# Optimization experiments

Measured on AMD Instinct MI355X. Metric: run time of the kernel, lower is better.

The kernel has to match this reference:

```python
import jax, jax.numpy as jnp
import numpy as np

D_MODEL = 1024
NUM_HEADS = 16
HEAD_DIM = D_MODEL // NUM_HEADS


def setup_inputs() -> dict:
    key = jax.random.key(0)
    ks = jax.random.split(key, 11)
    B, S = 2, 2048
    s = 1.0 / np.sqrt(D_MODEL)
    inp = {
        'q': jax.random.normal(ks[0], (B, S, D_MODEL), jnp.float32),
        'k': jax.random.normal(ks[1], (B, S, D_MODEL), jnp.float32),
        'v': jax.random.normal(ks[2], (B, S, D_MODEL), jnp.float32),
        'wq': jax.random.normal(ks[3], (D_MODEL, D_MODEL), jnp.float32) * s,
        'bq': jnp.zeros((D_MODEL,), jnp.float32),
        'wk': jax.random.normal(ks[4], (D_MODEL, D_MODEL), jnp.float32) * s,
        'bk': jnp.zeros((D_MODEL,), jnp.float32),
        'wv': jax.random.normal(ks[5], (D_MODEL, D_MODEL), jnp.float32) * s,
        'bv': jnp.zeros((D_MODEL,), jnp.float32),
        'wo': jax.random.normal(ks[6], (D_MODEL, D_MODEL), jnp.float32) * s,
        'bo': jnp.zeros((D_MODEL,), jnp.float32),
    }
    return inp


def _split_heads(x, B):
    # [B, S, D] -> [B, H, S, Hd]
    return x.reshape(B, -1, NUM_HEADS, HEAD_DIM).transpose(0, 2, 1, 3)


def reference(q, k, v, wq, bq, wk, bk, wv, bv, wo, bo):
    B = q.shape[0]
    qh = _split_heads(q @ wq + bq, B)
    kh = _split_heads(k @ wk + bk, B)
    vh = _split_heads(v @ wv + bv, B)
    scale = 1.0 / np.sqrt(HEAD_DIM).astype(np.float32)
    # [B, H, Sq, Sk]
    scores = jnp.einsum('bhqd,bhkd->bhqk', qh, kh) * scale
    probs = jax.nn.softmax(scores, axis=-1)
    out = jnp.einsum('bhqk,bhkd->bhqd', probs, vh)  # [B, H, Sq, Hd]
    out = out.transpose(0, 2, 1, 3).reshape(B, -1, D_MODEL)
    return out @ wo + bo
```

## Files before the change

### kernel.cpp

```cpp
#include <hip/hip_runtime.h>

typedef unsigned short u16;
typedef __bf16 bf16x8 __attribute__((ext_vector_type(8)));
typedef float    f32x4 __attribute__((ext_vector_type(4)));
typedef float   f32x16 __attribute__((ext_vector_type(16)));
typedef u16      u16x8 __attribute__((ext_vector_type(8)));
typedef u16      u16x4 __attribute__((ext_vector_type(4)));
typedef unsigned uint4v __attribute__((ext_vector_type(4)));

#define DM 1024
#define SQ 2048
#define HD 64
#define QSCALE 0.18033688f

#define SWZ8(row, ch) ((((ch) ^ ((row) & 7) ^ ((row) >> 3)) & 7))

__device__ __forceinline__ u16 f2bf(float f) {
    unsigned u = __builtin_bit_cast(unsigned, f);
    u += 0x7FFFu + ((u >> 16) & 1u);
    return (u16)(u >> 16);
}

__device__ __forceinline__ bf16x8 ldsbf(const u16* p) {
    return __builtin_bit_cast(bf16x8, *(const u16x8*)p);
}

__device__ __forceinline__ unsigned cvtpk(float a, float b) {
    unsigned r;
    asm("v_cvt_pk_bf16_f32 %0, %1, %2" : "=v"(r) : "v"(a), "v"(b));
    return r;
}

__device__ __forceinline__ void swap32(unsigned &a, unsigned &b) {
    asm volatile("v_permlane32_swap_b32 %0, %1" : "+v"(a), "+v"(b));
}

typedef __attribute__((address_space(3))) unsigned lds_u32_t;
typedef __attribute__((address_space(1))) const unsigned glob_u32_t;
__device__ __forceinline__ void gl_lds16(const u16* g, u16* l) {
    __builtin_amdgcn_global_load_lds((glob_u32_t*)g, (lds_u32_t*)l, 16, 0, 0);
}

__global__ __launch_bounds__(256) void prep_kernel(
    const float* __restrict__ q, const float* __restrict__ k,
    const float* __restrict__ v,
    const float* __restrict__ w0, const float* __restrict__ w1,
    const float* __restrict__ w2, const float* __restrict__ w3,
    u16* __restrict__ Qc, u16* __restrict__ Kc, u16* __restrict__ Vc,
    u16* __restrict__ t0, u16* __restrict__ t1,
    u16* __restrict__ t2, u16* __restrict__ t3)
{
    __shared__ float tile[32][33];
    const int bid = blockIdx.x;
    if (bid < 6144) {
        const int which = bid >> 11;
        const float* src = (which==0) ? q : (which==1) ? k : v;
        u16* dst         = (which==0) ? Qc : (which==1) ? Kc : Vc;
        const int off = ((bid & 2047) << 11) + threadIdx.x * 8;
        f32x4 x0 = *(const f32x4*)&src[off];
        f32x4 x1 = *(const f32x4*)&src[off + 4];
        u16x8 u;
#pragma unroll
        for (int e = 0; e < 4; ++e) { u[e] = f2bf(x0[e]); u[e+4] = f2bf(x1[e]); }
        *(u16x8*)&dst[off] = u;
    } else {
        const int t   = bid - 6144;
        const int z   = t >> 10;
        const int rem = t & 1023;
        const float* W = (z==0) ? w0 : (z==1) ? w1 : (z==2) ? w2 : w3;
        u16* T        = (z==0) ? t0 : (z==1) ? t1 : (z==2) ? t2 : t3;
        const float sc = (z==0) ? QSCALE : 1.0f;
        const int tx = threadIdx.x & 31, ty = threadIdx.x >> 5;
        const int n0 = (rem & 31) * 32, k0 = (rem >> 5) * 32;
#pragma unroll
        for (int i = 0; i < 4; ++i)
            tile[ty + 8*i][tx] = W[(size_t)(k0 + ty + 8*i)*DM + n0 + tx];
        __syncthreads();
#pragma unroll
        for (int i = 0; i < 4; ++i)
            T[(size_t)(n0 + ty + 8*i)*DM + k0 + tx] = f2bf(tile[tx][ty + 8*i] * sc);
    }
}

template<bool OF32, bool VTLAST>
__global__ __launch_bounds__(256) void gemm_kernel(
    const u16* __restrict__ a0, const u16* __restrict__ a1, const u16* __restrict__ a2,
    const u16* __restrict__ w0, const u16* __restrict__ w1, const u16* __restrict__ w2,
    const float* __restrict__ bi0, const float* __restrict__ bi1, const float* __restrict__ bi2,
    void* __restrict__ o0, void* __restrict__ o1, void* __restrict__ o2,
    float bscale0)
{
    __shared__ __align__(16) u16 As[2][128*64];
    __shared__ __align__(16) u16 Bs[2][128*64];

    const int cpx  = gridDim.x >> 3;
    const int wgid = (blockIdx.x & 7) * cpx + (blockIdx.x >> 3);
    const int z   = wgid >> 8;
    const int rem = wgid & 255;
    const int by  = rem >> 3, bx = rem & 7;

    const u16*  Ap  = (z==0) ? a0 : (z==1) ? a1 : a2;
    const u16*  Wp  = (z==0) ? w0 : (z==1) ? w1 : w2;
    const float* Bp = (z==0) ? bi0 : (z==1) ? bi1 : bi2;
    void* Op        = (z==0) ? o0 : (z==1) ? o1 : o2;
    const float bsc = (z==0) ? bscale0 : 1.0f;

    const int tid  = threadIdx.x;
    const int lane = tid & 63;
    const int wv   = tid >> 6;
    const int m0 = by * 128;
    const int n0 = bx * 128;
    const int wr = (wv >> 1) * 64;
    const int wc = (wv & 1) * 64;
    const int g  = lane >> 4;
    const int mm = lane & 15;

    const int l8 = lane >> 3;
    const int c8 = lane & 7;

    f32x4 acc[4][4];
#pragma unroll
    for (int i = 0; i < 4; ++i)
#pragma unroll
        for (int j = 0; j < 4; ++j) acc[i][j] = f32x4{0.f,0.f,0.f,0.f};

    auto stageA = [&](int kt, int buf) {
#pragma unroll
        for (int i = 0; i < 4; ++i) {
            const int row = i*32 + wv*8 + l8;
            const int ch  = c8 ^ (row & 7);
            gl_lds16(&Ap[(size_t)(m0+row)*DM + kt*64 + ch*8],
                     &As[buf][(i*32 + wv*8)*64]);
        }
    };
    auto stageW = [&](int kt, int buf) {
#pragma unroll
        for (int i = 0; i < 4; ++i) {
            const int row = i*32 + wv*8 + l8;
            const int ch  = c8 ^ (row & 7);
            gl_lds16(&Wp[(size_t)(n0+row)*DM + kt*64 + ch*8],
                     &Bs[buf][(i*32 + wv*8)*64]);
        }
    };

    stageA(0, 0); stageW(0, 0);

    for (int kt = 0; kt < 16; ++kt) {
        const int cur = kt & 1;
        if (kt < 15) { stageA(kt + 1, cur ^ 1); stageW(kt + 1, cur ^ 1); }
        if (kt < 15) asm volatile("s_waitcnt vmcnt(8)" ::: "memory");
        else         asm volatile("s_waitcnt vmcnt(0)" ::: "memory");
        __builtin_amdgcn_s_barrier();
        __builtin_amdgcn_sched_barrier(0);

#pragma unroll
        for (int ks = 0; ks < 2; ++ks) {
            bf16x8 af[4], bfr[4];
#pragma unroll
            for (int rt = 0; rt < 4; ++rt) {
                const int row = wr + rt*16 + mm;
                const int ch  = ks*4 + g;
                af[rt] = ldsbf(&As[cur][row*64 + ((ch ^ (row & 7)) << 3)]);
            }
#pragma unroll
            for (int ct = 0; ct < 4; ++ct) {
                const int row = wc + ct*16 + mm;
                const int ch  = ks*4 + g;
                bfr[ct] = ldsbf(&Bs[cur][row*64 + ((ch ^ (row & 7)) << 3)]);
            }
            __builtin_amdgcn_s_setprio(1);
#pragma unroll
            for (int rt = 0; rt < 4; ++rt)
#pragma unroll
                for (int ct = 0; ct < 4; ++ct)
                    acc[rt][ct] = __builtin_amdgcn_mfma_f32_16x16x32_bf16(
                        af[rt], bfr[ct], acc[rt][ct], 0, 0, 0);
            __builtin_amdgcn_s_setprio(0);
        }

        __builtin_amdgcn_sched_barrier(0);
        __builtin_amdgcn_s_barrier();
    }

    if (VTLAST && z == 2) {
#pragma unroll
        for (int ct = 0; ct < 4; ++ct) {
            const int col = n0 + wc + ct*16 + mm;
            const float bv = Bp[col] * bsc;
#pragma unroll
            for (int rt = 0; rt < 4; ++rt) {
                const int row0 = m0 + wr + rt*16 + g*4;
                const int bb = row0 >> 11, s = row0 & (SQ-1);
                u16x4 pk;
#pragma unroll
                for (int r = 0; r < 4; ++r) pk[r] = f2bf(acc[rt][ct][r] + bv);
                *(u16x4*)&((u16*)Op)[(size_t)(bb*DM + col)*SQ + s] = pk;
            }
        }
    } else {
#pragma unroll
        for (int ct = 0; ct < 4; ++ct) {
            const int col = n0 + wc + ct*16 + mm;
            const float bv = Bp[col] * bsc;
#pragma unroll
            for (int rt = 0; rt < 4; ++rt) {
#pragma unroll
                for (int r = 0; r < 4; ++r) {
                    const int row = m0 + wr + rt*16 + g*4 + r;
                    const float vv = acc[rt][ct][r] + bv;
                    if (OF32) ((float*)Op)[(size_t)row*DM + col] = vv;
                    else      ((u16*) Op)[(size_t)row*DM + col] = f2bf(vv);
                }
            }
        }
    }
}

__global__ __launch_bounds__(512) void attn_kernel(
    const u16* __restrict__ Q, const u16* __restrict__ K,
    const u16* __restrict__ Vt, u16* __restrict__ Z)
{
    __shared__ __align__(16) u16 Kl[2][64*64];
    __shared__ __align__(16) u16 Vl[2][64*64];

    const int tid  = threadIdx.x;
    const int lane = tid & 63;
    const int wid  = tid >> 6;
    const int c    = lane & 31;
    const int hi   = lane >> 5;
    const int srow = tid >> 3;
    const int c8   = tid & 7;

    const int wg = (blockIdx.x & 7) * 32 + (blockIdx.x >> 3);
    const int qt = wg & 7;
    const int hb = wg >> 3;
    const int h  = hb & 15;
    const int b  = hb >> 4;
    const int q0 = qt * 256;

    const size_t kbase = (size_t)(b*SQ)*DM + h*HD;
    const size_t vbase = (size_t)((b*16 + h)*HD)*SQ;

    bf16x8 qf[4];
    {
        const size_t qoff = (size_t)(b*SQ + q0 + wid*32 + c)*DM + h*HD + hi*8;
#pragma unroll
        for (int ks = 0; ks < 4; ++ks)
            qf[ks] = ldsbf(&Q[qoff + ks*16]);
    }

    f32x16 oacc[2];
#pragma unroll
    for (int dt = 0; dt < 2; ++dt)
#pragma unroll
        for (int r = 0; r < 16; ++r) oacc[dt][r] = 0.f;
    f32x16 z16;
#pragma unroll
    for (int r = 0; r < 16; ++r) z16[r] = 0.f;
    float lsp[4] = {0.f, 0.f, 0.f, 0.f};

    const int stw = srow*64 + (SWZ8(srow, c8) << 3);
    u16x8 kreg = *(const u16x8*)&K [kbase + (size_t)srow*DM + c8*8];
    u16x8 vreg = *(const u16x8*)&Vt[vbase + (size_t)srow*SQ + c8*8];
    *(u16x8*)&Kl[0][stw] = kreg;
    *(u16x8*)&Vl[0][stw] = vreg;

    for (int t = 0; t < SQ/64; ++t) {
        const int cur = t & 1;
        __syncthreads();
        if (t + 1 < SQ/64) {
            kreg = *(const u16x8*)&K [kbase + (size_t)((t+1)*64 + srow)*DM + c8*8];
            vreg = *(const u16x8*)&Vt[vbase + (size_t)srow*SQ + (t+1)*64 + c8*8];
        }

        f32x16 pacc[2];
        __builtin_amdgcn_s_setprio(1);
#pragma unroll
        for (int kt = 0; kt < 2; ++kt) {
            const int row = kt*32 + c;
            bf16x8 kf = ldsbf(&Kl[cur][row*64 + (SWZ8(row, hi) << 3)]);
            pacc[kt] = __builtin_amdgcn_mfma_f32_32x32x16_bf16(kf, qf[0], z16, 0, 0, 0);
        }
#pragma unroll
        for (int ks = 1; ks < 4; ++ks) {
#pragma unroll
            for (int kt = 0; kt < 2; ++kt) {
                const int row = kt*32 + c;
                const int ch  = ks*2 + hi;
                bf16x8 kf = ldsbf(&Kl[cur][row*64 + (SWZ8(row, ch) << 3)]);
                pacc[kt] = __builtin_amdgcn_mfma_f32_32x32x16_bf16(kf, qf[ks], pacc[kt], 0, 0, 0);
            }
        }
        __builtin_amdgcn_s_setprio(0);

#pragma unroll
        for (int kt = 0; kt < 2; ++kt)
#pragma unroll
            for (int r = 0; r < 16; ++r) {
                const float e = __builtin_amdgcn_exp2f(pacc[kt][r]);
                pacc[kt][r] = e;
                lsp[r & 3] += e;
            }

        bf16x8 pa[4];
#pragma unroll
        for (int kt = 0; kt < 2; ++kt)
#pragma unroll
            for (int k2 = 0; k2 < 2; ++k2) {
                const int bs = k2*8;
                unsigned u = cvtpk(pacc[kt][bs+0], pacc[kt][bs+1]);
                unsigned v = cvtpk(pacc[kt][bs+2], pacc[kt][bs+3]);
                unsigned w = cvtpk(pacc[kt][bs+4], pacc[kt][bs+5]);
                unsigned x = cvtpk(pacc[kt][bs+6], pacc[kt][bs+7]);
                swap32(u, w);
                swap32(v, x);
                uint4v fr = {u, v, w, x};
                pa[kt*2 + k2] = __builtin_bit_cast(bf16x8, fr);
            }

        __builtin_amdgcn_s_setprio(1);
#pragma unroll
        for (int kp = 0; kp < 4; ++kp) {
#pragma unroll
            for (int dt = 0; dt < 2; ++dt) {
                const int d  = dt*32 + c;
                const int ch = kp*2 + hi;
                bf16x8 vf = ldsbf(&Vl[cur][d*64 + (SWZ8(d, ch) << 3)]);
                oacc[dt] = __builtin_amdgcn_mfma_f32_32x32x16_bf16(pa[kp], vf, oacc[dt], 0, 0, 0);
            }
        }
        __builtin_amdgcn_s_setprio(0);

        if (t + 1 < SQ/64) {
            *(u16x8*)&Kl[cur^1][stw] = kreg;
            *(u16x8*)&Vl[cur^1][stw] = vreg;
        }
    }

    float lsum = (lsp[0] + lsp[1]) + (lsp[2] + lsp[3]);
    lsum += __shfl_xor(lsum, 32, 64);
    const float linv = 1.f / lsum;
    float linvr[16];
#pragma unroll
    for (int r = 0; r < 16; ++r)
        linvr[r] = __shfl(linv, (r & 3) + 8*(r >> 2) + 4*hi, 64);

#pragma unroll
    for (int dt = 0; dt < 2; ++dt)
#pragma unroll
        for (int r = 0; r < 16; ++r) {
            const int qrl = (r & 3) + 8*(r >> 2) + 4*hi;
            const size_t row = (size_t)(b*SQ + q0 + wid*32 + qrl);
            Z[row*DM + h*HD + dt*32 + c] = f2bf(oacc[dt][r] * linvr[r]);
        }
}

extern "C" void kernel_launch(void* const* d_in, const int* in_sizes, int n_in,
                              void* d_out, int out_size, void* d_ws, size_t ws_size,
                              hipStream_t stream)
{
    const float* q  = (const float*)d_in[0];
    const float* k  = (const float*)d_in[1];
    const float* v  = (const float*)d_in[2];
    const float* wq = (const float*)d_in[3];
    const float* bq = (const float*)d_in[4];
    const float* wk = (const float*)d_in[5];
    const float* bk = (const float*)d_in[6];
    const float* wv = (const float*)d_in[7];
    const float* bv = (const float*)d_in[8];
    const float* wo = (const float*)d_in[9];
    const float* bo = (const float*)d_in[10];
    float* out = (float*)d_out;

    char* ws = (char*)d_ws;
    u16* Qc  = (u16*)(ws);
    u16* Kc  = (u16*)(ws + 8388608);
    u16* Vc  = (u16*)(ws + 16777216);
    u16* Qb  = (u16*)(ws + 25165824);
    u16* Kb  = (u16*)(ws + 33554432);
    u16* VtB = (u16*)(ws + 41943040);
    u16* WtQ = (u16*)(ws + 50331648);
    u16* WtK = (u16*)(ws + 52428800);
    u16* WtV = (u16*)(ws + 54525952);
    u16* WtO = (u16*)(ws + 56623104);
    u16* Zb  = Qc;

    prep_kernel<<<dim3(6144 + 4096), 256, 0, stream>>>(
        q, k, v, wq, wk, wv, wo, Qc, Kc, Vc, WtQ, WtK, WtV, WtO);

    gemm_kernel<false, true><<<dim3(768), 256, 0, stream>>>(
        Qc, Kc, Vc, WtQ, WtK, WtV, bq, bk, bv,
        (void*)Qb, (void*)Kb, (void*)VtB, QSCALE);

    attn_kernel<<<dim3(256), 512, 0, stream>>>(Qb, Kb, VtB, Zb);

    gemm_kernel<true, false><<<dim3(256), 256, 0, stream>>>(
        Zb, Zb, Zb, WtO, WtO, WtO, bo, bo, bo,
        (void*)out, (void*)out, (void*)out, 1.0f);
}
```

Baseline: 116.6 us.

## Split attention KV range across two wave groups and reduce via LDS

```diff
diff --git a/kernel.cpp b/kernel.cpp
--- a/kernel.cpp
+++ b/kernel.cpp
@@ -216,34 +216,40 @@
     }
 }
 
-__global__ __launch_bounds__(512) void attn_kernel(
+__global__ __launch_bounds__(512, 4) void attn_kernel(
     const u16* __restrict__ Q, const u16* __restrict__ K,
     const u16* __restrict__ Vt, u16* __restrict__ Z)
 {
-    __shared__ __align__(16) u16 Kl[2][64*64];
-    __shared__ __align__(16) u16 Vl[2][64*64];
+    __shared__ __align__(16) u16 Kl[2][2][64*64];
+    __shared__ __align__(16) u16 Vl[2][2][64*64];
 
     const int tid  = threadIdx.x;
     const int lane = tid & 63;
     const int wid  = tid >> 6;
+    const int qw   = wid & 3;
+    const int st   = wid >> 2;
     const int c    = lane & 31;
     const int hi   = lane >> 5;
-    const int srow = tid >> 3;
-    const int c8   = tid & 7;
-
-    const int wg = (blockIdx.x & 7) * 32 + (blockIdx.x >> 3);
-    const int qt = wg & 7;
-    const int hb = wg >> 3;
+
+    const int g2   = tid & 255;
+    const int srow = g2 >> 2;
+    const int ch0  = g2 & 3;
+    const int ch1  = ch0 + 4;
+
+    const int wg = (blockIdx.x & 7) * 64 + (blockIdx.x >> 3);
+    const int qt = wg & 15;
+    const int hb = wg >> 4;
     const int h  = hb & 15;
     const int b  = hb >> 4;
-    const int q0 = qt * 256;
+    const int q0 = qt * 128;
 
     const size_t kbase = (size_t)(b*SQ)*DM + h*HD;
     const size_t vbase = (size_t)((b*16 + h)*HD)*SQ;
+    const int    kv0   = st * 1024;
 
     bf16x8 qf[4];
     {
-        const size_t qoff = (size_t)(b*SQ + q0 + wid*32 + c)*DM + h*HD + hi*8;
+        const size_t qoff = (size_t)(b*SQ + q0 + qw*32 + c)*DM + h*HD + hi*8;
 #pragma unroll
         for (int ks = 0; ks < 4; ++ks)
             qf[ks] = ldsbf(&Q[qoff + ks*16]);
@@ -259,18 +265,29 @@
     for (int r = 0; r < 16; ++r) z16[r] = 0.f;
     float lsp[4] = {0.f, 0.f, 0.f, 0.f};
 
-    const int stw = srow*64 + (SWZ8(srow, c8) << 3);
-    u16x8 kreg = *(const u16x8*)&K [kbase + (size_t)srow*DM + c8*8];
-    u16x8 vreg = *(const u16x8*)&Vt[vbase + (size_t)srow*SQ + c8*8];
-    *(u16x8*)&Kl[0][stw] = kreg;
-    *(u16x8*)&Vl[0][stw] = vreg;
-
-    for (int t = 0; t < SQ/64; ++t) {
+    const int stw0 = srow*64 + (SWZ8(srow, ch0) << 3);
+    const int stw1 = srow*64 + (SWZ8(srow, ch1) << 3);
+    u16x8 kr0, kr1, vr0, vr1;
+    kr0 = *(const u16x8*)&K [kbase + (size_t)(kv0 + srow)*DM + ch0*8];
+    kr1 = *(const u16x8*)&K [kbase + (size_t)(kv0 + srow)*DM + ch1*8];
+    vr0 = *(const u16x8*)&Vt[vbase + (size_t)srow*SQ + kv0 + ch0*8];
+    vr1 = *(const u16x8*)&Vt[vbase + (size_t)srow*SQ + kv0 + ch1*8];
+    *(u16x8*)&Kl[st][0][stw0] = kr0;
+    *(u16x8*)&Kl[st][0][stw1] = kr1;
+    *(u16x8*)&Vl[st][0][stw0] = vr0;
+    *(u16x8*)&Vl[st][0][stw1] = vr1;
+
+    const int NT = 16;
+    for (int t = 0; t < NT; ++t) {
         const int cur = t & 1;
         __syncthreads();
-        if (t + 1 < SQ/64) {
-            kreg = *(const u16x8*)&K [kbase + (size_t)((t+1)*64 + srow)*DM + c8*8];
-            vreg = *(const u16x8*)&Vt[vbase + (size_t)srow*SQ + (t+1)*64 + c8*8];
+        if (t + 1 < NT) {
+            const size_t krow = kbase + (size_t)(kv0 + (t+1)*64 + srow)*DM;
+            const size_t vrow = vbase + (size_t)srow*SQ + kv0 + (t+1)*64;
+            kr0 = *(const u16x8*)&K [krow + ch0*8];
+            kr1 = *(const u16x8*)&K [krow + ch1*8];
+            vr0 = *(const u16x8*)&Vt[vrow + ch0*8];
+            vr1 = *(const u16x8*)&Vt[vrow + ch1*8];
         }
 
         f32x16 pacc[2];
@@ -278,7 +295,7 @@
 #pragma unroll
         for (int kt = 0; kt < 2; ++kt) {
             const int row = kt*32 + c;
-            bf16x8 kf = ldsbf(&Kl[cur][row*64 + (SWZ8(row, hi) << 3)]);
+            bf16x8 kf = ldsbf(&Kl[st][cur][row*64 + (SWZ8(row, hi) << 3)]);
             pacc[kt] = __builtin_amdgcn_mfma_f32_32x32x16_bf16(kf, qf[0], z16, 0, 0, 0);
         }
 #pragma unroll
@@ -287,7 +304,7 @@
             for (int kt = 0; kt < 2; ++kt) {
                 const int row = kt*32 + c;
                 const int ch  = ks*2 + hi;
-                bf16x8 kf = ldsbf(&Kl[cur][row*64 + (SWZ8(row, ch) << 3)]);
+                bf16x8 kf = ldsbf(&Kl[st][cur][row*64 + (SWZ8(row, ch) << 3)]);
                 pacc[kt] = __builtin_amdgcn_mfma_f32_32x32x16_bf16(kf, qf[ks], pacc[kt], 0, 0, 0);
             }
         }
@@ -325,34 +342,57 @@
             for (int dt = 0; dt < 2; ++dt) {
                 const int d  = dt*32 + c;
                 const int ch = kp*2 + hi;
-                bf16x8 vf = ldsbf(&Vl[cur][d*64 + (SWZ8(d, ch) << 3)]);
+                bf16x8 vf = ldsbf(&Vl[st][cur][d*64 + (SWZ8(d, ch) << 3)]);
                 oacc[dt] = __builtin_amdgcn_mfma_f32_32x32x16_bf16(pa[kp], vf, oacc[dt], 0, 0, 0);
             }
         }
         __builtin_amdgcn_s_setprio(0);
 
-        if (t + 1 < SQ/64) {
-            *(u16x8*)&Kl[cur^1][stw] = kreg;
-            *(u16x8*)&Vl[cur^1][stw] = vreg;
+        if (t + 1 < NT) {
+            *(u16x8*)&Kl[st][cur^1][stw0] = kr0;
+            *(u16x8*)&Kl[st][cur^1][stw1] = kr1;
+            *(u16x8*)&Vl[st][cur^1][stw0] = vr0;
+            *(u16x8*)&Vl[st][cur^1][stw1] = vr1;
         }
     }
 
     float lsum = (lsp[0] + lsp[1]) + (lsp[2] + lsp[3]);
-    lsum += __shfl_xor(lsum, 32, 64);
-    const float linv = 1.f / lsum;
-    float linvr[16];
-#pragma unroll
-    for (int r = 0; r < 16; ++r)
-        linvr[r] = __shfl(linv, (r & 3) + 8*(r >> 2) + 4*hi, 64);
-
-#pragma unroll
-    for (int dt = 0; dt < 2; ++dt)
+    float* sc = (float*)&Kl[0][0][0];
+    __syncthreads();
+    if (st == 1) {
+        const int base = (qw*64 + lane)*33;
 #pragma unroll
         for (int r = 0; r < 16; ++r) {
-            const int qrl = (r & 3) + 8*(r >> 2) + 4*hi;
-            const size_t row = (size_t)(b*SQ + q0 + wid*32 + qrl);
-            Z[row*DM + h*HD + dt*32 + c] = f2bf(oacc[dt][r] * linvr[r]);
-        }
+            sc[base + r]      = oacc[0][r];
+            sc[base + 16 + r] = oacc[1][r];
+        }
+        sc[base + 32] = lsum;
+    }
+    __syncthreads();
+    if (st == 0) {
+        const int base = (qw*64 + lane)*33;
+#pragma unroll
+        for (int r = 0; r < 16; ++r) {
+            oacc[0][r] += sc[base + r];
+            oacc[1][r] += sc[base + 16 + r];
+        }
+        lsum += sc[base + 32];
+        lsum += __shfl_xor(lsum, 32, 64);
+        const float linv = 1.f / lsum;
+        float linvr[16];
+#pragma unroll
+        for (int r = 0; r < 16; ++r)
+            linvr[r] = __shfl(linv, (r & 3) + 8*(r >> 2) + 4*hi, 64);
+
+#pragma unroll
+        for (int dt = 0; dt < 2; ++dt)
+#pragma unroll
+            for (int r = 0; r < 16; ++r) {
+                const int qrl = (r & 3) + 8*(r >> 2) + 4*hi;
+                const size_t row = (size_t)(b*SQ + q0 + qw*32 + qrl);
+                Z[row*DM + h*HD + dt*32 + c] = f2bf(oacc[dt][r] * linvr[r]);
+            }
+    }
 }
 
 extern "C" void kernel_launch(void* const* d_in, const int* in_sizes, int n_in,
@@ -392,7 +432,7 @@
         Qc, Kc, Vc, WtQ, WtK, WtV, bq, bk, bv,
         (void*)Qb, (void*)Kb, (void*)VtB, QSCALE);
 
-    attn_kernel<<<dim3(256), 512, 0, stream>>>(Qb, Kb, VtB, Zb);
+    attn_kernel<<<dim3(512), 512, 0, stream>>>(Qb, Kb, VtB, Zb);
 
     gemm_kernel<true, false><<<dim3(256), 256, 0, stream>>>(
         Zb, Zb, Zb, WtO, WtO, WtO, bo, bo, bo,
```

Measured after the change: 124.8 us. 7.1% more time.

## Stage K/V tiles with direct global-to-LDS loads in attention loop

Applied to the files above, without the earlier changes.

```diff
diff --git a/kernel.cpp b/kernel.cpp
--- a/kernel.cpp
+++ b/kernel.cpp
@@ -259,19 +259,22 @@
     for (int r = 0; r < 16; ++r) z16[r] = 0.f;
     float lsp[4] = {0.f, 0.f, 0.f, 0.f};
 
-    const int stw = srow*64 + (SWZ8(srow, c8) << 3);
-    u16x8 kreg = *(const u16x8*)&K [kbase + (size_t)srow*DM + c8*8];
-    u16x8 vreg = *(const u16x8*)&Vt[vbase + (size_t)srow*SQ + c8*8];
-    *(u16x8*)&Kl[0][stw] = kreg;
-    *(u16x8*)&Vl[0][stw] = vreg;
-
-    for (int t = 0; t < SQ/64; ++t) {
+    const int sc = SWZ8(srow, c8);
+    auto stage = [&](int t, int buf) {
+        gl_lds16(&K [kbase + (size_t)(t*64 + srow)*DM + sc*8], &Kl[buf][wid*512]);
+        gl_lds16(&Vt[vbase + (size_t)srow*SQ + t*64 + sc*8],   &Vl[buf][wid*512]);
+    };
+
+    stage(0, 0);
+
+    const int NT = SQ/64;
+    for (int t = 0; t < NT; ++t) {
         const int cur = t & 1;
-        __syncthreads();
-        if (t + 1 < SQ/64) {
-            kreg = *(const u16x8*)&K [kbase + (size_t)((t+1)*64 + srow)*DM + c8*8];
-            vreg = *(const u16x8*)&Vt[vbase + (size_t)srow*SQ + (t+1)*64 + c8*8];
-        }
+        if (t + 1 < NT) stage(t + 1, cur ^ 1);
+        if (t + 1 < NT) asm volatile("s_waitcnt vmcnt(2)" ::: "memory");
+        else            asm volatile("s_waitcnt vmcnt(0)" ::: "memory");
+        __builtin_amdgcn_s_barrier();
+        __builtin_amdgcn_sched_barrier(0);
 
         f32x16 pacc[2];
         __builtin_amdgcn_s_setprio(1);
@@ -331,10 +334,8 @@
         }
         __builtin_amdgcn_s_setprio(0);
 
-        if (t + 1 < SQ/64) {
-            *(u16x8*)&Kl[cur^1][stw] = kreg;
-            *(u16x8*)&Vl[cur^1][stw] = vreg;
-        }
+        __builtin_amdgcn_sched_barrier(0);
+        __builtin_amdgcn_s_barrier();
     }
 
     float lsum = (lsp[0] + lsp[1]) + (lsp[2] + lsp[3]);
```

New measurement: 123.5 us. +5.9%, slower.
